# Kernel tuning notes

Hardware: AMD Instinct MI355X
Metric: run time of the kernel (lower is better)

## Reference

```python
import jax, jax.numpy as jnp
import numpy as np

ORDER = 16
FRAME = 160
EPS = 1e-8


def setup_inputs() -> dict:
    key = jax.random.key(0)
    B, T = 64, 320000  # 64 utterances x 20s @ 16kHz; T % FRAME == 0
    x = jax.random.normal(key, (B, T), dtype=jnp.float32)
    return {"x": x}


def _lpc_residual(x):
    # x: [B, T] -> residual [B, T, 1]
    B, T = x.shape
    F = T // FRAME
    frm = x.reshape(B, F, FRAME)  # [B, F, 160]

    # Autocorrelation lags 0..ORDER (equiv. np.correlate(frm, frm, 'full')[160-1 : 160+16])
    r = jnp.stack(
        [jnp.sum(frm[..., : FRAME - k] * frm[..., k:], axis=-1) for k in range(ORDER + 1)],
        axis=-1,
    )  # [B, F, 17]

    # Levinson-Durbin recursion, batched over (B, F); loop over fixed small ORDER.
    a = jnp.zeros((B, F, ORDER + 1), dtype=x.dtype).at[..., 0].set(1.0)
    e = jnp.where(r[..., 0] != 0, r[..., 0], EPS)
    for i in range(1, ORDER + 1):
        # acc = r[i] - sum_{j=1}^{i-1} a[j] * r[i-j]
        acc = r[..., i] - jnp.sum(a[..., 1:i] * r[..., 1:i][..., ::-1], axis=-1)
        safe_e = jnp.where(e != 0, e, 1.0)
        k = jnp.where(e != 0, acc / safe_e, 0.0)
        a_new = a[..., 1:i] - k[..., None] * a[..., i - 1:0:-1]
        a = a.at[..., 1:i].set(a_new)
        a = a.at[..., i].set(k)
        e = jnp.maximum(e * (1.0 - k * k), EPS)

    # FIR filter: lfilter(a, [1.0], frm) -> res[n] = sum_k a[k] * frm[n-k] (zero-padded)
    res = a[..., 0:1] * frm
    for k in range(1, ORDER + 1):
        shifted = jnp.pad(frm, ((0, 0), (0, 0), (k, 0)))[..., :FRAME]
        res = res + a[..., k:k + 1] * shifted

    return res.reshape(B, T)[..., None]


def reference(x):
    return _lpc_residual(x)
```

## Files before the change

kernel.cpp:

```cpp
#include <hip/hip_runtime.h>

#define FRAME 160
#define ORDER 16
#define LPC_EPS 1e-8f
#define NF 32
#define BS 256
#define SEG 20
#define SX 164
#define QPB (NF * FRAME / 4 / BS)

__global__ __launch_bounds__(BS, 4) void lpc_fused(const float* __restrict__ x,
                                                   float* __restrict__ out) {
    __shared__ float xs[NF * SX];

    const int t = threadIdx.x;
    const long long base = (long long)blockIdx.x * (NF * FRAME);

#pragma unroll
    for (int it = 0; it < QPB; ++it) {
        int p = it * BS + t;
        int f = p / 40;
        int off = (p - f * 40) * 4;
        float4 v = *(const float4*)(x + base + 4 * p);
        *(float4*)(&xs[f * SX + off]) = v;
    }
    __syncthreads();

    const int fi = t >> 3;
    const int part = t & 7;
    const int sbase = SEG * part;

    float w[SEG + ORDER];
#pragma unroll
    for (int m = 0; m < (SEG + ORDER) / 4; ++m) {
        int idx = sbase + 4 * m;
        float4 v = make_float4(0.f, 0.f, 0.f, 0.f);
        if (idx < FRAME) v = *(const float4*)(&xs[fi * SX + idx]);
        w[4 * m + 0] = v.x; w[4 * m + 1] = v.y;
        w[4 * m + 2] = v.z; w[4 * m + 3] = v.w;
    }

    float r[ORDER + 1];
#pragma unroll
    for (int k = 0; k <= ORDER; ++k) r[k] = 0.f;
#pragma unroll
    for (int n = 0; n < SEG; ++n) {
#pragma unroll
        for (int k = 0; k <= ORDER; ++k) {
            r[k] = fmaf(w[n], w[n + k], r[k]);
        }
    }
#pragma unroll
    for (int k = 0; k <= ORDER; ++k) {
        r[k] += __shfl_xor(r[k], 1);
        r[k] += __shfl_xor(r[k], 2);
        r[k] += __shfl_xor(r[k], 4);
    }

    float a[ORDER + 1];
    a[0] = 1.f;
#pragma unroll
    for (int j = 1; j <= ORDER; ++j) a[j] = 0.f;
    float e = (r[0] != 0.f) ? r[0] : LPC_EPS;
#pragma unroll
    for (int i = 1; i <= ORDER; ++i) {
        float acc = r[i];
#pragma unroll
        for (int j = 1; j < i; ++j) acc -= a[j] * r[i - j];
        float k = acc / e;
#pragma unroll
        for (int j = 1; 2 * j < i; ++j) {
            float aj = a[j], aij = a[i - j];
            a[j]     = aj  - k * aij;
            a[i - j] = aij - k * aj;
        }
        if ((i & 1) == 0) {
            int m = i >> 1;
            a[m] = a[m] - k * a[m];
        }
        a[i] = k;
        e = fmaxf(e * (1.f - k * k), LPC_EPS);
    }

    float pre[ORDER];
#pragma unroll
    for (int m = 0; m < ORDER / 4; ++m) {
        int idx = sbase - ORDER + 4 * m;
        float4 v = make_float4(0.f, 0.f, 0.f, 0.f);
        if (idx >= 0) v = *(const float4*)(&xs[fi * SX + idx]);
        pre[4 * m + 0] = v.x; pre[4 * m + 1] = v.y;
        pre[4 * m + 2] = v.z; pre[4 * m + 3] = v.w;
    }

    __syncthreads();

#pragma unroll
    for (int m = 0; m < SEG / 4; ++m) {
        float o[4];
#pragma unroll
        for (int i = 0; i < 4; ++i) {
            int n = 4 * m + i;
            float s = 0.f;
#pragma unroll
            for (int k = 0; k <= ORDER; ++k) {
                int j = n - k;
                float xv = (j >= 0) ? w[j] : pre[ORDER + j];
                s = fmaf(a[k], xv, s);
            }
            o[i] = s;
        }
        *(float4*)(&xs[fi * SX + sbase + 4 * m]) = make_float4(o[0], o[1], o[2], o[3]);
    }
    __syncthreads();

#pragma unroll
    for (int it = 0; it < QPB; ++it) {
        int p = it * BS + t;
        int f = p / 40;
        int off = (p - f * 40) * 4;
        float4 v = *(const float4*)(&xs[f * SX + off]);
        *(float4*)(out + base + 4 * p) = v;
    }
}

extern "C" void kernel_launch(void* const* d_in, const int* in_sizes, int n_in,
                              void* d_out, int out_size, void* d_ws, size_t ws_size,
                              hipStream_t stream) {
    const float* x = (const float*)d_in[0];
    float* out = (float*)d_out;
    int total = in_sizes[0];
    int n_frames = total / FRAME;
    int n_blocks = n_frames / NF;
    lpc_fused<<<n_blocks, BS, 0, stream>>>(x, out);
}
```

Baseline: 40.77 us.

## Run Levinson-Durbin once per frame in one thread and share coefficients via LDS

```diff
diff --git a/kernel.cpp b/kernel.cpp
--- a/kernel.cpp
+++ b/kernel.cpp
@@ -7,11 +7,14 @@
 #define BS 256
 #define SEG 20
 #define SX 164
+#define AB 20
 #define QPB (NF * FRAME / 4 / BS)
 
 __global__ __launch_bounds__(BS, 4) void lpc_fused(const float* __restrict__ x,
                                                    float* __restrict__ out) {
     __shared__ float xs[NF * SX];
+    __shared__ float rbuf[NF * AB];
+    __shared__ float abuf[NF * AB];
 
     const int t = threadIdx.x;
     const long long base = (long long)blockIdx.x * (NF * FRAME);
@@ -40,6 +43,16 @@
         w[4 * m + 2] = v.z; w[4 * m + 3] = v.w;
     }
 
+    float pre[ORDER];
+#pragma unroll
+    for (int m = 0; m < ORDER / 4; ++m) {
+        int idx = sbase - ORDER + 4 * m;
+        float4 v = make_float4(0.f, 0.f, 0.f, 0.f);
+        if (idx >= 0) v = *(const float4*)(&xs[fi * SX + idx]);
+        pre[4 * m + 0] = v.x; pre[4 * m + 1] = v.y;
+        pre[4 * m + 2] = v.z; pre[4 * m + 3] = v.w;
+    }
+
     float r[ORDER + 1];
 #pragma unroll
     for (int k = 0; k <= ORDER; ++k) r[k] = 0.f;
@@ -57,42 +70,64 @@
         r[k] += __shfl_xor(r[k], 4);
     }
 
+    if (part == 0) {
+#pragma unroll
+        for (int m = 0; m < 4; ++m)
+            *(float4*)(&rbuf[fi * AB + 4 * m]) =
+                make_float4(r[4 * m], r[4 * m + 1], r[4 * m + 2], r[4 * m + 3]);
+        rbuf[fi * AB + 16] = r[16];
+    }
+    __syncthreads();
+
+    if (t < NF) {
+        float rr[ORDER + 1];
+#pragma unroll
+        for (int m = 0; m < 4; ++m) {
+            float4 v = *(const float4*)(&rbuf[t * AB + 4 * m]);
+            rr[4 * m + 0] = v.x; rr[4 * m + 1] = v.y;
+            rr[4 * m + 2] = v.z; rr[4 * m + 3] = v.w;
+        }
+        rr[16] = rbuf[t * AB + 16];
+
+        float a[ORDER + 1];
+        a[0] = 1.f;
+#pragma unroll
+        for (int j = 1; j <= ORDER; ++j) a[j] = 0.f;
+        float e = (rr[0] != 0.f) ? rr[0] : LPC_EPS;
+#pragma unroll
+        for (int i = 1; i <= ORDER; ++i) {
+            float acc = rr[i];
+#pragma unroll
+            for (int j = 1; j < i; ++j) acc -= a[j] * rr[i - j];
+            float k = acc * __builtin_amdgcn_rcpf(e);
+#pragma unroll
+            for (int j = 1; 2 * j < i; ++j) {
+                float aj = a[j], aij = a[i - j];
+                a[j]     = aj  - k * aij;
+                a[i - j] = aij - k * aj;
+            }
+            if ((i & 1) == 0) {
+                int m = i >> 1;
+                a[m] = a[m] - k * a[m];
+            }
+            a[i] = k;
+            e = fmaxf(e * (1.f - k * k), LPC_EPS);
+        }
+#pragma unroll
+        for (int m = 0; m < 4; ++m)
+            *(float4*)(&abuf[t * AB + 4 * m]) =
+                make_float4(a[4 * m + 1], a[4 * m + 2], a[4 * m + 3], a[4 * m + 4]);
+    }
+    __syncthreads();
+
     float a[ORDER + 1];
     a[0] = 1.f;
 #pragma unroll
-    for (int j = 1; j <= ORDER; ++j) a[j] = 0.f;
-    float e = (r[0] != 0.f) ? r[0] : LPC_EPS;
-#pragma unroll
-    for (int i = 1; i <= ORDER; ++i) {
-        float acc = r[i];
-#pragma unroll
-        for (int j = 1; j < i; ++j) acc -= a[j] * r[i - j];
-        float k = acc / e;
-#pragma unroll
-        for (int j = 1; 2 * j < i; ++j) {
-            float aj = a[j], aij = a[i - j];
-            a[j]     = aj  - k * aij;
-            a[i - j] = aij - k * aj;
-        }
-        if ((i & 1) == 0) {
-            int m = i >> 1;
-            a[m] = a[m] - k * a[m];
-        }
-        a[i] = k;
-        e = fmaxf(e * (1.f - k * k), LPC_EPS);
+    for (int m = 0; m < 4; ++m) {
+        float4 v = *(const float4*)(&abuf[fi * AB + 4 * m]);
+        a[4 * m + 1] = v.x; a[4 * m + 2] = v.y;
+        a[4 * m + 3] = v.z; a[4 * m + 4] = v.w;
     }
-
-    float pre[ORDER];
-#pragma unroll
-    for (int m = 0; m < ORDER / 4; ++m) {
-        int idx = sbase - ORDER + 4 * m;
-        float4 v = make_float4(0.f, 0.f, 0.f, 0.f);
-        if (idx >= 0) v = *(const float4*)(&xs[fi * SX + idx]);
-        pre[4 * m + 0] = v.x; pre[4 * m + 1] = v.y;
-        pre[4 * m + 2] = v.z; pre[4 * m + 3] = v.w;
-    }
-
-    __syncthreads();
 
 #pragma unroll
     for (int m = 0; m < SEG / 4; ++m) {
```

New measurement: 39.75 us. 2.5% less time.
